# Kernel tuning notes

Hardware: AMD Instinct MI355X
Metric: run time of the kernel (lower is better)

Reference implementation:

```python
import jax, jax.numpy as jnp
import numpy as np

D_MODEL = 1024
N_HEADS = 16
D_K = D_MODEL // N_HEADS


def setup_inputs() -> dict:
    key = jax.random.key(0)
    ks = jax.random.split(key, 12)
    B, S = 2, 2048
    scale = 1.0 / np.sqrt(D_MODEL)
    inp = {
        "q": jax.random.normal(ks[0], (B, S, D_MODEL), jnp.float32),
        "k": jax.random.normal(ks[1], (B, S, D_MODEL), jnp.float32),
        "v": jax.random.normal(ks[2], (B, S, D_MODEL), jnp.float32),
        "k_pe": jax.random.normal(ks[3], (N_HEADS, D_K, S), jnp.float32),
        "Wq": jax.random.normal(ks[4], (D_MODEL, D_MODEL), jnp.float32) * scale,
        "bq": jnp.zeros((D_MODEL,), jnp.float32),
        "Wk": jax.random.normal(ks[5], (D_MODEL, D_MODEL), jnp.float32) * scale,
        "bk": jnp.zeros((D_MODEL,), jnp.float32),
        "Wv": jax.random.normal(ks[6], (D_MODEL, D_MODEL), jnp.float32) * scale,
        "bv": jnp.zeros((D_MODEL,), jnp.float32),
        "Wo": jax.random.normal(ks[7], (D_MODEL, D_MODEL), jnp.float32) * scale,
        "bo": jnp.zeros((D_MODEL,), jnp.float32),
    }
    return inp


def reference(q, k, v, k_pe, Wq, bq, Wk, bk, Wv, bv, Wo, bo):
    B, S, _ = q.shape
    # projections -> [B, H, S, d_k]
    def split_heads(x):
        return x.reshape(B, S, N_HEADS, D_K).transpose(0, 2, 1, 3)
    qh = split_heads(q @ Wq + bq)
    kh = split_heads(k @ Wk + bk)
    vh = split_heads(v @ Wv + bv)
    # content scores + relative positional scores (two matmuls, summed)
    scores = jnp.einsum("bhsd,bhtd->bhst", qh, kh)
    scores = scores + jnp.einsum("bhsd,hdt->bhst", qh, k_pe)
    scores = scores / jnp.sqrt(jnp.asarray(D_K, qh.dtype))
    attn = jax.nn.softmax(scores, axis=-1)
    out = jnp.einsum("bhst,bhtd->bhsd", attn, vh)  # [B,H,S,d_k]
    out = out.transpose(0, 2, 1, 3).reshape(B, S, D_MODEL)
    return out @ Wo + bo
```

## Files before the change

kernel.cpp:

```cpp
#include <hip/hip_runtime.h>
#include <stdint.h>
#include <math.h>

typedef __bf16 bf16;
typedef __attribute__((ext_vector_type(8))) __bf16 bf16x8;
typedef __attribute__((ext_vector_type(4))) __bf16 bf16x4;
typedef __attribute__((ext_vector_type(4))) float f32x4;

#define MFMA_BF16(a, b, c) __builtin_amdgcn_mfma_f32_16x16x32_bf16((a), (b), (c), 0, 0, 0)

#if __has_builtin(__builtin_amdgcn_exp2f)
#define EXP2F __builtin_amdgcn_exp2f
#else
#define EXP2F exp2f
#endif

#define QSCALE 0.18033688011112042f

__device__ __forceinline__ void gl_lds16(const bf16* g, bf16* l) {
  __builtin_amdgcn_global_load_lds(
      (__attribute__((address_space(1))) unsigned int*)(uintptr_t)(g),
      (__attribute__((address_space(3))) unsigned int*)(l),
      16, 0, 0);
}

__global__ __launch_bounds__(256) void prep(
    const float* __restrict__ q, const float* __restrict__ k,
    const float* __restrict__ v, bf16* __restrict__ qb,
    bf16* __restrict__ kb, bf16* __restrict__ vb,
    const float* __restrict__ W0, const float* __restrict__ W1,
    const float* __restrict__ W2, const float* __restrict__ W3,
    bf16* __restrict__ Wt,
    const float* __restrict__ kpe, bf16* __restrict__ kpeb)
{
  __shared__ float tile[64][65];
  const int tid = threadIdx.x;
  const int bid = blockIdx.x;
  if (bid < 6144) {
    const int z = bid >> 11;
    const int idx = bid & 2047;
    const float* s = (z == 0) ? q : (z == 1) ? k : v;
    bf16* d = (z == 0) ? qb : (z == 1) ? kb : vb;
    size_t i = ((size_t)idx * 256 + tid) * 8;
    float4 a = *(const float4*)(s + i);
    float4 b = *(const float4*)(s + i + 4);
    bf16x8 o;
    o[0] = (bf16)a.x; o[1] = (bf16)a.y; o[2] = (bf16)a.z; o[3] = (bf16)a.w;
    o[4] = (bf16)b.x; o[5] = (bf16)b.y; o[6] = (bf16)b.z; o[7] = (bf16)b.w;
    *(bf16x8*)(d + i) = o;
  } else if (bid < 7168) {
    const int t = bid - 6144;
    const int z = t >> 8;
    const int rem = t & 255;
    const int r0 = (rem >> 4) * 64, c0 = (rem & 15) * 64;
    const float* src = (z == 0) ? W0 : (z == 1) ? W1 : (z == 2) ? W2 : W3;
    bf16* dst = Wt + (size_t)z * (1024 * 1024);
#pragma unroll
    for (int h = 0; h < 2; ++h) {
      int qq = tid + h * 256;
      int row = qq >> 3, cc = qq & 7;
      float4 a = *(const float4*)(src + (size_t)(r0 + row) * 1024 + c0 + cc * 8);
      float4 b = *(const float4*)(src + (size_t)(r0 + row) * 1024 + c0 + cc * 8 + 4);
      tile[row][cc * 8 + 0] = a.x; tile[row][cc * 8 + 1] = a.y;
      tile[row][cc * 8 + 2] = a.z; tile[row][cc * 8 + 3] = a.w;
      tile[row][cc * 8 + 4] = b.x; tile[row][cc * 8 + 5] = b.y;
      tile[row][cc * 8 + 6] = b.z; tile[row][cc * 8 + 7] = b.w;
    }
    __syncthreads();
#pragma unroll
    for (int h = 0; h < 2; ++h) {
      int qq = tid + h * 256;
      int row = qq >> 3, cc = qq & 7;
      bf16x8 o;
#pragma unroll
      for (int e = 0; e < 8; ++e) o[e] = (bf16)tile[cc * 8 + e][row];
      *(bf16x8*)(dst + (size_t)(c0 + row) * 1024 + r0 + cc * 8) = o;
    }
  } else {
    const int idx = bid - 7168;
    size_t i = ((size_t)idx * 256 + tid) * 8;
    float4 a = *(const float4*)(kpe + i);
    float4 b = *(const float4*)(kpe + i + 4);
    bf16x8 o;
    o[0] = (bf16)a.x; o[1] = (bf16)a.y; o[2] = (bf16)a.z; o[3] = (bf16)a.w;
    o[4] = (bf16)b.x; o[5] = (bf16)b.y; o[6] = (bf16)b.z; o[7] = (bf16)b.w;
    *(bf16x8*)(kpeb + i) = o;
  }
}

template <int MODE>
__device__ __forceinline__ void gemm_body(
    const bf16* __restrict__ A, const bf16* __restrict__ Wt,
    const float* __restrict__ bias, float oscale,
    const bf16* __restrict__ kpeb, void* __restrict__ out_v,
    bf16* __restrict__ As, bf16* __restrict__ Bs)
{
  const int tid = threadIdx.x;
  const int w = tid >> 6, lane = tid & 63;
  const int lm = lane & 15, quad = lane >> 4;
  const int wr = w >> 1, wc = w & 1;
  const int m0 = blockIdx.y * 128, n0 = blockIdx.x * 128;

  f32x4 zero4 = {0.f, 0.f, 0.f, 0.f};
  f32x4 acc[4][4];
#pragma unroll
  for (int i = 0; i < 4; ++i)
#pragma unroll
    for (int j = 0; j < 4; ++j) acc[i][j] = zero4;

  auto stage = [&](int buf, int kb) {
#pragma unroll
    for (int h = 0; h < 2; ++h) {
      int qq = tid + h * 256;
      int row = qq >> 2, cs = qq & 3;
      int cc = cs ^ ((row >> 1) & 3);
      gl_lds16(A + (size_t)(m0 + row) * 1024 + kb * 32 + cc * 8,
               As + buf * 4096 + qq * 8);
      gl_lds16(Wt + (size_t)(n0 + row) * 1024 + kb * 32 + cc * 8,
               Bs + buf * 4096 + qq * 8);
    }
  };

  stage(0, 0);
  __syncthreads();

  int cur = 0;
  for (int kb = 0; kb < 32; ++kb) {
    if (kb < 31) stage(cur ^ 1, kb + 1);

    const bf16* Ab = As + cur * 4096;
    const bf16* Bb = Bs + cur * 4096;
    bf16x8 af[4], bfv[4];
#pragma unroll
    for (int i = 0; i < 4; ++i) {
      int row = wr * 64 + i * 16 + lm;
      af[i] = *(const bf16x8*)(Ab + row * 32 + ((quad ^ ((row >> 1) & 3)) * 8));
    }
#pragma unroll
    for (int j = 0; j < 4; ++j) {
      int row = wc * 64 + j * 16 + lm;
      bfv[j] = *(const bf16x8*)(Bb + row * 32 + ((quad ^ ((row >> 1) & 3)) * 8));
    }
#pragma unroll
    for (int i = 0; i < 4; ++i)
#pragma unroll
      for (int j = 0; j < 4; ++j)
        acc[i][j] = MFMA_BF16(af[i], bfv[j], acc[i][j]);

    __syncthreads();
    cur ^= 1;
  }

  const int ncol = n0 + wc * 64;
  float bv4[4];
#pragma unroll
  for (int j = 0; j < 4; ++j) bv4[j] = bias[ncol + j * 16 + lm];
#pragma unroll
  for (int i = 0; i < 4; ++i) {
    const int mbase = m0 + wr * 64 + i * 16 + quad * 4;
    const int b = mbase >> 11, s = mbase & 2047;
#pragma unroll
    for (int j = 0; j < 4; ++j) {
      const int ng = ncol + j * 16 + lm;
      const int hh = ng >> 6, d = ng & 63;
      if (MODE == 2) {
        bf16x4 o;
#pragma unroll
        for (int r = 0; r < 4; ++r) o[r] = (bf16)(acc[i][j][r] + bv4[j]);
        *(bf16x4*)((bf16*)out_v + ((size_t)(b * 16 + hh) * 64 + d) * 2048 + s) = o;
      } else if (MODE == 1) {
        bf16x4 p4 = *(const bf16x4*)(kpeb + ((size_t)(hh * 64 + d)) * 2048 + s);
#pragma unroll
        for (int r = 0; r < 4; ++r) {
          float val = acc[i][j][r] + bv4[j] + (float)p4[r];
          ((bf16*)out_v)[(((size_t)(b * 16 + hh)) * 2048 + (s + r)) * 64 + d] =
              (bf16)val;
        }
      } else if (MODE == 0) {
#pragma unroll
        for (int r = 0; r < 4; ++r) {
          float val = acc[i][j][r] + bv4[j];
          ((bf16*)out_v)[(((size_t)(b * 16 + hh)) * 2048 + (s + r)) * 64 + d] =
              (bf16)(val * oscale);
        }
      } else {
#pragma unroll
        for (int r = 0; r < 4; ++r) {
          float val = acc[i][j][r] + bv4[j];
          ((float*)out_v)[(size_t)(mbase + r) * 1024 + ng] = val;
        }
      }
    }
  }
}

__global__ __launch_bounds__(256) void qkv_gemm(
    const bf16* __restrict__ qb, const bf16* __restrict__ kb, const bf16* __restrict__ vb,
    const bf16* __restrict__ Wt, const float* __restrict__ biq,
    const float* __restrict__ bik, const float* __restrict__ biv,
    const bf16* __restrict__ kpeb,
    bf16* __restrict__ Qs, bf16* __restrict__ Ks, bf16* __restrict__ Vts)
{
  __shared__ __align__(16) bf16 As[2 * 128 * 32];
  __shared__ __align__(16) bf16 Bs[2 * 128 * 32];
  const int z = blockIdx.z;
  if (z == 0) {
    gemm_body<0>(qb, Wt, biq, QSCALE, nullptr, Qs, As, Bs);
  } else if (z == 1) {
    gemm_body<1>(kb, Wt + (size_t)1 * 1024 * 1024, bik, 1.f, kpeb, Ks, As, Bs);
  } else {
    gemm_body<2>(vb, Wt + (size_t)2 * 1024 * 1024, biv, 1.f, nullptr, Vts, As, Bs);
  }
}

__global__ __launch_bounds__(256) void out_gemm(
    const bf16* __restrict__ A, const bf16* __restrict__ Wt,
    const float* __restrict__ bias, float* __restrict__ out)
{
  __shared__ __align__(16) bf16 As[2 * 128 * 32];
  __shared__ __align__(16) bf16 Bs[2 * 128 * 32];
  gemm_body<3>(A, Wt, bias, 1.f, nullptr, out, As, Bs);
}

__global__ __launch_bounds__(512) void flash_attn(
    const bf16* __restrict__ Q, const bf16* __restrict__ K,
    const bf16* __restrict__ Vt, bf16* __restrict__ O)
{
  __shared__ __align__(16) bf16 QtPs[128 * 72];
  __shared__ __align__(16) bf16 Kt[2][64 * 64];
  __shared__ __align__(16) bf16 Vs[2][64 * 64];
  bf16* Ps = QtPs;

  const int tid = threadIdx.x;
  const int w = tid >> 6, lane = tid & 63;
  const int lm = lane & 15, quad = lane >> 4;
  const int bh = blockIdx.y;
  const int s0 = blockIdx.x * 128;
  const size_t qkbase = (size_t)bh * (2048 * 64);
  const size_t vbase = (size_t)bh * (64 * 2048);

#pragma unroll
  for (int h = 0; h < 2; ++h) {
    int qq = tid + h * 512;
    int row = qq >> 3, cs = qq & 7;
    int cc = cs ^ (row & 7);
    gl_lds16(Q + qkbase + (size_t)(s0 + row) * 64 + cc * 8, QtPs + qq * 8);
  }
  {
    int row = tid >> 3, cs = tid & 7;
    int cc = cs ^ (row & 7);
    gl_lds16(K + qkbase + (size_t)row * 64 + cc * 8, Kt[0] + tid * 8);
    gl_lds16(Vt + vbase + (size_t)row * 2048 + cc * 8, Vs[0] + tid * 8);
  }
  __syncthreads();

  bf16x8 qa0, qa1;
  {
    int row = w * 16 + lm;
    qa0 = *(const bf16x8*)(QtPs + row * 64 + ((quad ^ (row & 7)) * 8));
    qa1 = *(const bf16x8*)(QtPs + row * 64 + (((quad + 4) ^ (row & 7)) * 8));
  }
  __syncthreads();

  f32x4 zero4 = {0.f, 0.f, 0.f, 0.f};
  float l_part = 0.f;
  f32x4 oacc[4];
#pragma unroll
  for (int dt = 0; dt < 4; ++dt) oacc[dt] = zero4;

  const int prow = (w * 16 + lm) * 72;

  for (int kt = 0; kt < 32; ++kt) {
    const int cur = kt & 1;
    if (kt < 31) {
      const int t1 = (kt + 1) * 64;
      int row = tid >> 3, cs = tid & 7;
      int cc = cs ^ (row & 7);
      gl_lds16(K + qkbase + (size_t)(t1 + row) * 64 + cc * 8, Kt[cur ^ 1] + tid * 8);
      gl_lds16(Vt + vbase + (size_t)row * 2048 + t1 + cc * 8, Vs[cur ^ 1] + tid * 8);
    }

#pragma unroll
    for (int c = 0; c < 4; ++c) {
      int row = c * 16 + lm;
      bf16x8 kb0 = *(const bf16x8*)(Kt[cur] + row * 64 + ((quad ^ (row & 7)) * 8));
      bf16x8 kb1 = *(const bf16x8*)(Kt[cur] + row * 64 + (((quad + 4) ^ (row & 7)) * 8));
      __builtin_amdgcn_s_setprio(1);
      f32x4 z = MFMA_BF16(kb0, qa0, zero4);
      f32x4 st = MFMA_BF16(kb1, qa1, z);
      __builtin_amdgcn_s_setprio(0);
      bf16x4 pk;
#pragma unroll
      for (int r = 0; r < 4; ++r) {
        float p = EXP2F(st[r]);
        l_part += p;
        pk[r] = (bf16)p;
      }
      *(bf16x4*)(Ps + prow + c * 16 + quad * 4) = pk;
    }

    bf16x8 pa0 = *(const bf16x8*)(Ps + prow + quad * 8);
    bf16x8 pa1 = *(const bf16x8*)(Ps + prow + 32 + quad * 8);
#pragma unroll
    for (int dt = 0; dt < 4; ++dt) {
      int row = dt * 16 + lm;
      bf16x8 va0 = *(const bf16x8*)(Vs[cur] + row * 64 + ((quad ^ (row & 7)) * 8));
      bf16x8 va1 = *(const bf16x8*)(Vs[cur] + row * 64 + (((quad + 4) ^ (row & 7)) * 8));
      __builtin_amdgcn_s_setprio(1);
      oacc[dt] = MFMA_BF16(va0, pa0, oacc[dt]);
      oacc[dt] = MFMA_BF16(va1, pa1, oacc[dt]);
      __builtin_amdgcn_s_setprio(0);
    }

    __syncthreads();
  }

  float l = l_part;
  l += __shfl_xor(l, 16, 64);
  l += __shfl_xor(l, 32, 64);
  float inv = 1.f / l;
#pragma unroll
  for (int dt = 0; dt < 4; ++dt)
#pragma unroll
    for (int r = 0; r < 4; ++r)
      Ps[prow + dt * 16 + quad * 4 + r] = (bf16)(oacc[dt][r] * inv);

  const int b = bh >> 4, hh = bh & 15;
  const int srow = s0 + w * 16 + lm;
  const size_t ob = ((size_t)(b * 2048 + srow)) * 1024 + hh * 64;
#pragma unroll
  for (int half = 0; half < 2; ++half) {
    bf16x8 ov = *(const bf16x8*)(Ps + prow + (half * 4 + quad) * 8);
    *(bf16x8*)(O + ob + (half * 4 + quad) * 8) = ov;
  }
}

extern "C" void kernel_launch(void* const* d_in, const int* in_sizes, int n_in,
                              void* d_out, int out_size, void* d_ws, size_t ws_size,
                              hipStream_t stream) {
  (void)in_sizes; (void)n_in; (void)out_size; (void)ws_size;
  const float* q   = (const float*)d_in[0];
  const float* k   = (const float*)d_in[1];
  const float* v   = (const float*)d_in[2];
  const float* kpe = (const float*)d_in[3];
  const float* Wq  = (const float*)d_in[4];
  const float* bq  = (const float*)d_in[5];
  const float* Wk  = (const float*)d_in[6];
  const float* bk  = (const float*)d_in[7];
  const float* Wv  = (const float*)d_in[8];
  const float* bv  = (const float*)d_in[9];
  const float* Wo  = (const float*)d_in[10];
  const float* bo  = (const float*)d_in[11];

  const size_t NT = 4u * 1024 * 1024;
  bf16* ws  = (bf16*)d_ws;
  bf16* Wt  = ws;
  bf16* qb  = Wt + NT;
  bf16* kb  = qb + NT;
  bf16* vb  = kb + NT;
  bf16* Qs  = vb + NT;
  bf16* Ks  = Qs + NT;
  bf16* Vts = Ks + NT;
  bf16* Oa  = Vts + NT;
  bf16* kpeb = Oa;

  prep<<<dim3(8192), 256, 0, stream>>>(q, k, v, qb, kb, vb, Wq, Wk, Wv, Wo, Wt,
                                       kpe, kpeb);
  qkv_gemm<<<dim3(8, 32, 3), 256, 0, stream>>>(qb, kb, vb, Wt, bq, bk, bv, kpeb,
                                               Qs, Ks, Vts);
  flash_attn<<<dim3(16, 32), 512, 0, stream>>>(Qs, Ks, Vts, Oa);
  out_gemm<<<dim3(8, 32), 256, 0, stream>>>(Oa, Wt + 3u * 1024 * 1024, bo,
                                            (float*)d_out);
}
```

Measured before the change: 243.2 us.

## Fuse fp32-to-bf16 activation conversion into QKV GEMM A-tile loads

Drops the prep pass that converted q, k and v from fp32 to bf16 in global memory. The QKV GEMM now stages the fp32 A tiles straight into LDS with an XOR swizzle and converts to bf16 when building MFMA fragments. This removes a full write and re-read of three activation tensors, at the cost of doubling A-tile LDS footprint and global read bytes per K step, which could lower occupancy. kpeb also moves to its own workspace slot instead of aliasing Oa.

```diff
diff --git a/kernel.cpp b/kernel.cpp
--- a/kernel.cpp
+++ b/kernel.cpp
@@ -17,7 +17,7 @@
 
 #define QSCALE 0.18033688011112042f
 
-__device__ __forceinline__ void gl_lds16(const bf16* g, bf16* l) {
+__device__ __forceinline__ void gl_lds16(const void* g, void* l) {
   __builtin_amdgcn_global_load_lds(
       (__attribute__((address_space(1))) unsigned int*)(uintptr_t)(g),
       (__attribute__((address_space(3))) unsigned int*)(l),
@@ -25,9 +25,6 @@
 }
 
 __global__ __launch_bounds__(256) void prep(
-    const float* __restrict__ q, const float* __restrict__ k,
-    const float* __restrict__ v, bf16* __restrict__ qb,
-    bf16* __restrict__ kb, bf16* __restrict__ vb,
     const float* __restrict__ W0, const float* __restrict__ W1,
     const float* __restrict__ W2, const float* __restrict__ W3,
     bf16* __restrict__ Wt,
@@ -36,20 +33,8 @@
   __shared__ float tile[64][65];
   const int tid = threadIdx.x;
   const int bid = blockIdx.x;
-  if (bid < 6144) {
-    const int z = bid >> 11;
-    const int idx = bid & 2047;
-    const float* s = (z == 0) ? q : (z == 1) ? k : v;
-    bf16* d = (z == 0) ? qb : (z == 1) ? kb : vb;
-    size_t i = ((size_t)idx * 256 + tid) * 8;
-    float4 a = *(const float4*)(s + i);
-    float4 b = *(const float4*)(s + i + 4);
-    bf16x8 o;
-    o[0] = (bf16)a.x; o[1] = (bf16)a.y; o[2] = (bf16)a.z; o[3] = (bf16)a.w;
-    o[4] = (bf16)b.x; o[5] = (bf16)b.y; o[6] = (bf16)b.z; o[7] = (bf16)b.w;
-    *(bf16x8*)(d + i) = o;
-  } else if (bid < 7168) {
-    const int t = bid - 6144;
+  if (bid < 1024) {
+    const int t = bid;
     const int z = t >> 8;
     const int rem = t & 255;
     const int r0 = (rem >> 4) * 64, c0 = (rem & 15) * 64;
@@ -77,7 +62,7 @@
       *(bf16x8*)(dst + (size_t)(c0 + row) * 1024 + r0 + cc * 8) = o;
     }
   } else {
-    const int idx = bid - 7168;
+    const int idx = bid - 1024;
     size_t i = ((size_t)idx * 256 + tid) * 8;
     float4 a = *(const float4*)(kpe + i);
     float4 b = *(const float4*)(kpe + i + 4);
@@ -88,12 +73,12 @@
   }
 }
 
-template <int MODE>
+template <int MODE, bool AF32>
 __device__ __forceinline__ void gemm_body(
-    const bf16* __restrict__ A, const bf16* __restrict__ Wt,
+    const void* __restrict__ A_, const bf16* __restrict__ Wt,
     const float* __restrict__ bias, float oscale,
     const bf16* __restrict__ kpeb, void* __restrict__ out_v,
-    bf16* __restrict__ As, bf16* __restrict__ Bs)
+    void* __restrict__ As_, bf16* __restrict__ Bs)
 {
   const int tid = threadIdx.x;
   const int w = tid >> 6, lane = tid & 63;
@@ -109,13 +94,32 @@
     for (int j = 0; j < 4; ++j) acc[i][j] = zero4;
 
   auto stage = [&](int buf, int kb) {
+    if (AF32) {
+      const float* A = (const float*)A_;
+#pragma unroll
+      for (int h = 0; h < 4; ++h) {
+        int qq = tid + h * 256;
+        int row = qq >> 3, cs = qq & 7;
+        int cc = cs ^ (row & 7);
+        gl_lds16(A + (size_t)(m0 + row) * 1024 + kb * 32 + cc * 4,
+                 (float*)As_ + buf * 4096 + qq * 4);
+      }
+    } else {
+      const bf16* A = (const bf16*)A_;
+#pragma unroll
+      for (int h = 0; h < 2; ++h) {
+        int qq = tid + h * 256;
+        int row = qq >> 2, cs = qq & 3;
+        int cc = cs ^ ((row >> 1) & 3);
+        gl_lds16(A + (size_t)(m0 + row) * 1024 + kb * 32 + cc * 8,
+                 (bf16*)As_ + buf * 4096 + qq * 8);
+      }
+    }
 #pragma unroll
     for (int h = 0; h < 2; ++h) {
       int qq = tid + h * 256;
       int row = qq >> 2, cs = qq & 3;
       int cc = cs ^ ((row >> 1) & 3);
-      gl_lds16(A + (size_t)(m0 + row) * 1024 + kb * 32 + cc * 8,
-               As + buf * 4096 + qq * 8);
       gl_lds16(Wt + (size_t)(n0 + row) * 1024 + kb * 32 + cc * 8,
                Bs + buf * 4096 + qq * 8);
     }
@@ -128,14 +132,30 @@
   for (int kb = 0; kb < 32; ++kb) {
     if (kb < 31) stage(cur ^ 1, kb + 1);
 
-    const bf16* Ab = As + cur * 4096;
+    bf16x8 af[4], bfv[4];
+    if (AF32) {
+      const float* Ab = (const float*)As_ + cur * 4096;
+#pragma unroll
+      for (int i = 0; i < 4; ++i) {
+        int row = wr * 64 + i * 16 + lm;
+        const float* Ar = Ab + row * 32;
+        int r7 = row & 7;
+        float4 fa = *(const float4*)(Ar + (((2 * quad) ^ r7) * 4));
+        float4 fb = *(const float4*)(Ar + (((2 * quad + 1) ^ r7) * 4));
+        bf16x8 v;
+        v[0] = (bf16)fa.x; v[1] = (bf16)fa.y; v[2] = (bf16)fa.z; v[3] = (bf16)fa.w;
+        v[4] = (bf16)fb.x; v[5] = (bf16)fb.y; v[6] = (bf16)fb.z; v[7] = (bf16)fb.w;
+        af[i] = v;
+      }
+    } else {
+      const bf16* Ab = (const bf16*)As_ + cur * 4096;
+#pragma unroll
+      for (int i = 0; i < 4; ++i) {
+        int row = wr * 64 + i * 16 + lm;
+        af[i] = *(const bf16x8*)(Ab + row * 32 + ((quad ^ ((row >> 1) & 3)) * 8));
+      }
+    }
     const bf16* Bb = Bs + cur * 4096;
-    bf16x8 af[4], bfv[4];
-#pragma unroll
-    for (int i = 0; i < 4; ++i) {
-      int row = wr * 64 + i * 16 + lm;
-      af[i] = *(const bf16x8*)(Ab + row * 32 + ((quad ^ ((row >> 1) & 3)) * 8));
-    }
 #pragma unroll
     for (int j = 0; j < 4; ++j) {
       int row = wc * 64 + j * 16 + lm;
@@ -195,21 +215,21 @@
 }
 
 __global__ __launch_bounds__(256) void qkv_gemm(
-    const bf16* __restrict__ qb, const bf16* __restrict__ kb, const bf16* __restrict__ vb,
+    const float* __restrict__ q, const float* __restrict__ k, const float* __restrict__ v,
     const bf16* __restrict__ Wt, const float* __restrict__ biq,
     const float* __restrict__ bik, const float* __restrict__ biv,
     const bf16* __restrict__ kpeb,
     bf16* __restrict__ Qs, bf16* __restrict__ Ks, bf16* __restrict__ Vts)
 {
-  __shared__ __align__(16) bf16 As[2 * 128 * 32];
+  __shared__ __align__(16) float Asf[2 * 128 * 32];
   __shared__ __align__(16) bf16 Bs[2 * 128 * 32];
   const int z = blockIdx.z;
   if (z == 0) {
-    gemm_body<0>(qb, Wt, biq, QSCALE, nullptr, Qs, As, Bs);
+    gemm_body<0, true>(q, Wt, biq, QSCALE, nullptr, Qs, Asf, Bs);
   } else if (z == 1) {
-    gemm_body<1>(kb, Wt + (size_t)1 * 1024 * 1024, bik, 1.f, kpeb, Ks, As, Bs);
+    gemm_body<1, true>(k, Wt + (size_t)1 * 1024 * 1024, bik, 1.f, kpeb, Ks, Asf, Bs);
   } else {
-    gemm_body<2>(vb, Wt + (size_t)2 * 1024 * 1024, biv, 1.f, nullptr, Vts, As, Bs);
+    gemm_body<2, true>(v, Wt + (size_t)2 * 1024 * 1024, biv, 1.f, nullptr, Vts, Asf, Bs);
   }
 }
 
@@ -219,7 +239,7 @@
 {
   __shared__ __align__(16) bf16 As[2 * 128 * 32];
   __shared__ __align__(16) bf16 Bs[2 * 128 * 32];
-  gemm_body<3>(A, Wt, bias, 1.f, nullptr, out, As, Bs);
+  gemm_body<3, false>(A, Wt, bias, 1.f, nullptr, out, As, Bs);
 }
 
 __global__ __launch_bounds__(512) void flash_attn(
@@ -355,18 +375,14 @@
   const size_t NT = 4u * 1024 * 1024;
   bf16* ws  = (bf16*)d_ws;
   bf16* Wt  = ws;
-  bf16* qb  = Wt + NT;
-  bf16* kb  = qb + NT;
-  bf16* vb  = kb + NT;
-  bf16* Qs  = vb + NT;
+  bf16* Qs  = Wt + NT;
   bf16* Ks  = Qs + NT;
   bf16* Vts = Ks + NT;
   bf16* Oa  = Vts + NT;
-  bf16* kpeb = Oa;
-
-  prep<<<dim3(8192), 256, 0, stream>>>(q, k, v, qb, kb, vb, Wq, Wk, Wv, Wo, Wt,
-                                       kpe, kpeb);
-  qkv_gemm<<<dim3(8, 32, 3), 256, 0, stream>>>(qb, kb, vb, Wt, bq, bk, bv, kpeb,
+  bf16* kpeb = Oa + NT;
+
+  prep<<<dim3(2048), 256, 0, stream>>>(Wq, Wk, Wv, Wo, Wt, kpe, kpeb);
+  qkv_gemm<<<dim3(8, 32, 3), 256, 0, stream>>>(q, k, v, Wt, bq, bk, bv, kpeb,
                                                Qs, Ks, Vts);
   flash_attn<<<dim3(16, 32), 512, 0, stream>>>(Qs, Ks, Vts, Oa);
   out_gemm<<<dim3(8, 32), 256, 0, stream>>>(Oa, Wt + 3u * 1024 * 1024, bo,
```

Measured after the change: 292.7 us. 20.4% more time.

## Triple-buffer GEMM LDS staging with vmcnt waits and XCD-aware tile remap

Applied to the files above, without the earlier changes.

The shared GEMM body now uses three LDS buffers and prefetches two k-blocks ahead. It replaces __syncthreads with partial s_waitcnt vmcnt plus raw barriers, so global-to-LDS loads stay in flight across iterations. Block indices are also remapped so that consecutive blocks on the same XCD share M tiles, which should improve L2 reuse. The cost is more LDS per block, which may reduce occupancy, and the hand-written vmcnt counts depend on exactly four loads being issued per stage.

```diff
diff --git a/kernel.cpp b/kernel.cpp
--- a/kernel.cpp
+++ b/kernel.cpp
@@ -99,14 +99,17 @@
   const int w = tid >> 6, lane = tid & 63;
   const int lm = lane & 15, quad = lane >> 4;
   const int wr = w >> 1, wc = w & 1;
-  const int m0 = blockIdx.y * 128, n0 = blockIdx.x * 128;
+  const int lid = blockIdx.x + (blockIdx.y << 3);
+  const int xcd = lid & 7, j = lid >> 3;
+  const int m0 = (xcd * 4 + (j & 3)) * 128;
+  const int n0 = (j >> 2) * 128;
 
   f32x4 zero4 = {0.f, 0.f, 0.f, 0.f};
   f32x4 acc[4][4];
 #pragma unroll
   for (int i = 0; i < 4; ++i)
 #pragma unroll
-    for (int j = 0; j < 4; ++j) acc[i][j] = zero4;
+    for (int jj = 0; jj < 4; ++jj) acc[i][jj] = zero4;
 
   auto stage = [&](int buf, int kb) {
 #pragma unroll
@@ -122,11 +125,20 @@
   };
 
   stage(0, 0);
-  __syncthreads();
+  stage(1, 1);
 
   int cur = 0;
   for (int kb = 0; kb < 32; ++kb) {
-    if (kb < 31) stage(cur ^ 1, kb + 1);
+    if (kb < 30) {
+      stage((kb + 2) % 3, kb + 2);
+      asm volatile("s_waitcnt vmcnt(8)" ::: "memory");
+    } else if (kb == 30) {
+      asm volatile("s_waitcnt vmcnt(4)" ::: "memory");
+    } else {
+      asm volatile("s_waitcnt vmcnt(0)" ::: "memory");
+    }
+    __builtin_amdgcn_s_barrier();
+    asm volatile("" ::: "memory");
 
     const bf16* Ab = As + cur * 4096;
     const bf16* Bb = Bs + cur * 4096;
@@ -137,56 +149,57 @@
       af[i] = *(const bf16x8*)(Ab + row * 32 + ((quad ^ ((row >> 1) & 3)) * 8));
     }
 #pragma unroll
-    for (int j = 0; j < 4; ++j) {
-      int row = wc * 64 + j * 16 + lm;
-      bfv[j] = *(const bf16x8*)(Bb + row * 32 + ((quad ^ ((row >> 1) & 3)) * 8));
+    for (int jj = 0; jj < 4; ++jj) {
+      int row = wc * 64 + jj * 16 + lm;
+      bfv[jj] = *(const bf16x8*)(Bb + row * 32 + ((quad ^ ((row >> 1) & 3)) * 8));
     }
 #pragma unroll
     for (int i = 0; i < 4; ++i)
 #pragma unroll
-      for (int j = 0; j < 4; ++j)
-        acc[i][j] = MFMA_BF16(af[i], bfv[j], acc[i][j]);
-
-    __syncthreads();
-    cur ^= 1;
+      for (int jj = 0; jj < 4; ++jj)
+        acc[i][jj] = MFMA_BF16(af[i], bfv[jj], acc[i][jj]);
+
+    __builtin_amdgcn_s_barrier();
+    asm volatile("" ::: "memory");
+    cur = (cur + 1) == 3 ? 0 : cur + 1;
   }
 
   const int ncol = n0 + wc * 64;
   float bv4[4];
 #pragma unroll
-  for (int j = 0; j < 4; ++j) bv4[j] = bias[ncol + j * 16 + lm];
+  for (int jj = 0; jj < 4; ++jj) bv4[jj] = bias[ncol + jj * 16 + lm];
 #pragma unroll
   for (int i = 0; i < 4; ++i) {
     const int mbase = m0 + wr * 64 + i * 16 + quad * 4;
     const int b = mbase >> 11, s = mbase & 2047;
 #pragma unroll
-    for (int j = 0; j < 4; ++j) {
-      const int ng = ncol + j * 16 + lm;
+    for (int jj = 0; jj < 4; ++jj) {
+      const int ng = ncol + jj * 16 + lm;
       const int hh = ng >> 6, d = ng & 63;
       if (MODE == 2) {
         bf16x4 o;
 #pragma unroll
-        for (int r = 0; r < 4; ++r) o[r] = (bf16)(acc[i][j][r] + bv4[j]);
+        for (int r = 0; r < 4; ++r) o[r] = (bf16)(acc[i][jj][r] + bv4[jj]);
         *(bf16x4*)((bf16*)out_v + ((size_t)(b * 16 + hh) * 64 + d) * 2048 + s) = o;
       } else if (MODE == 1) {
         bf16x4 p4 = *(const bf16x4*)(kpeb + ((size_t)(hh * 64 + d)) * 2048 + s);
 #pragma unroll
         for (int r = 0; r < 4; ++r) {
-          float val = acc[i][j][r] + bv4[j] + (float)p4[r];
+          float val = acc[i][jj][r] + bv4[jj] + (float)p4[r];
           ((bf16*)out_v)[(((size_t)(b * 16 + hh)) * 2048 + (s + r)) * 64 + d] =
               (bf16)val;
         }
       } else if (MODE == 0) {
 #pragma unroll
         for (int r = 0; r < 4; ++r) {
-          float val = acc[i][j][r] + bv4[j];
+          float val = acc[i][jj][r] + bv4[jj];
           ((bf16*)out_v)[(((size_t)(b * 16 + hh)) * 2048 + (s + r)) * 64 + d] =
               (bf16)(val * oscale);
         }
       } else {
 #pragma unroll
         for (int r = 0; r < 4; ++r) {
-          float val = acc[i][j][r] + bv4[j];
+          float val = acc[i][jj][r] + bv4[jj];
           ((float*)out_v)[(size_t)(mbase + r) * 1024 + ng] = val;
         }
       }
@@ -201,8 +214,8 @@
     const bf16* __restrict__ kpeb,
     bf16* __restrict__ Qs, bf16* __restrict__ Ks, bf16* __restrict__ Vts)
 {
-  __shared__ __align__(16) bf16 As[2 * 128 * 32];
-  __shared__ __align__(16) bf16 Bs[2 * 128 * 32];
+  __shared__ __align__(16) bf16 As[3 * 128 * 32];
+  __shared__ __align__(16) bf16 Bs[3 * 128 * 32];
   const int z = blockIdx.z;
   if (z == 0) {
     gemm_body<0>(qb, Wt, biq, QSCALE, nullptr, Qs, As, Bs);
@@ -217,8 +230,8 @@
     const bf16* __restrict__ A, const bf16* __restrict__ Wt,
     const float* __restrict__ bias, float* __restrict__ out)
 {
-  __shared__ __align__(16) bf16 As[2 * 128 * 32];
-  __shared__ __align__(16) bf16 Bs[2 * 128 * 32];
+  __shared__ __align__(16) bf16 As[3 * 128 * 32];
+  __shared__ __align__(16) bf16 Bs[3 * 128 * 32];
   gemm_body<3>(A, Wt, bias, 1.f, nullptr, out, As, Bs);
 }
 
```

Result: no change. 241.1 us (-0.8%).
